# Kernel tuning notes

Hardware: AMD Instinct MI355X
Metric: run time of the kernel (lower is better)

## Reference

```python
import jax, jax.numpy as jnp
import numpy as np
import math

N_EMBD = 384
N_HEAD = 6
HEAD_DIM = N_EMBD // N_HEAD  # 64
EPS = 1e-5


def apply_rotary_emb(x, cos, sin):
    # x: [B, T, H, D]; cos/sin: [1, T, 1, D//2]
    d = x.shape[3] // 2
    x1, x2 = x[..., :d], x[..., d:]
    y1 = x1 * cos + x2 * sin
    y2 = -x1 * sin + x2 * cos
    return jnp.concatenate([y1, y2], axis=3).astype(x.dtype)


def rms_norm(x):
    # no learned gain, eps inside the sqrt's argument as in the torch code
    return x * jax.lax.rsqrt(jnp.mean(x * x, axis=-1, keepdims=True) + EPS)


def setup_inputs() -> dict:
    key = jax.random.key(0)
    ks = jax.random.split(key, 7)
    B, T = 8, 2048
    x = jax.random.normal(ks[0], (B, T, N_EMBD), dtype=jnp.float32)
    scale = 1.0 / math.sqrt(N_EMBD)
    Wq = jax.random.normal(ks[1], (N_EMBD, N_EMBD), dtype=jnp.float32) * scale
    Wk = jax.random.normal(ks[2], (N_EMBD, N_EMBD), dtype=jnp.float32) * scale
    Wv = jax.random.normal(ks[3], (N_EMBD, N_EMBD), dtype=jnp.float32) * scale
    Wo = jax.random.normal(ks[4], (N_EMBD, N_EMBD), dtype=jnp.float32) * scale
    # RoPE tables: true cos/sin of position*inv_freq
    half = HEAD_DIM // 2
    inv_freq = 1.0 / (10000.0 ** (jnp.arange(half, dtype=jnp.float32) / half))
    t = jnp.arange(T, dtype=jnp.float32)
    freqs = t[:, None] * inv_freq[None, :]  # [T, half]
    cos = jnp.cos(freqs)[None, :, None, :]  # [1, T, 1, half]
    sin = jnp.sin(freqs)[None, :, None, :]
    return {"x": x, "Wq": Wq, "Wk": Wk, "Wv": Wv, "Wo": Wo, "cos": cos, "sin": sin}


def reference(x, Wq, Wk, Wv, Wo, cos, sin):
    B, T, C = x.shape
    H, D = N_HEAD, HEAD_DIM
    # torch Linear: y = x @ W.T (weights stored [out, in])
    q = (x @ Wq.T).reshape(B, T, H, D)
    k = (x @ Wk.T).reshape(B, T, H, D)
    v = (x @ Wv.T).reshape(B, T, H, D)
    q = apply_rotary_emb(q, cos, sin)
    k = apply_rotary_emb(k, cos, sin)
    q = rms_norm(q)
    k = rms_norm(k)
    # attention: [B, H, T, T] scores, full softmax (no causal mask in source)
    att = jnp.einsum("bthd,bshd->bhts", q, k) * (1.0 / math.sqrt(D))
    att = jax.nn.softmax(att, axis=-1)
    y = jnp.einsum("bhts,bshd->bthd", att, v).reshape(B, T, C)
    return y @ Wo.T
```

## Files before the change

### kernel.cpp

```cpp
#include <hip/hip_runtime.h>
#include <hip/hip_bf16.h>
#include <stdint.h>

#define B_ 8
#define T_ 2048
#define C_ 384
#define H_ 6
#define D_ 64
#define M_ (B_*T_)

typedef unsigned short u16;
typedef unsigned int u32;
typedef __attribute__((ext_vector_type(8))) short short8;
typedef __attribute__((ext_vector_type(4))) float floatx4;
typedef __attribute__((ext_vector_type(16))) float floatx16;

#define QSCALE 0.18033688011112042f

__device__ __forceinline__ u16 f2b(float f) {
  union { float f; unsigned u; } x; x.f = f;
  unsigned r = x.u + 0x7fffu + ((x.u >> 16) & 1u);
  return (u16)(r >> 16);
}
__device__ __forceinline__ u32 pack_bf16(float a, float b) {
  union { __hip_bfloat162 h; u32 u; } x;
  x.h = __float22bfloat162_rn(float2{a, b});
  return x.u;
}
__device__ __forceinline__ uint4 pack8(const float4& lo, const float4& hi) {
  uint4 r;
  r.x = pack_bf16(lo.x, lo.y); r.y = pack_bf16(lo.z, lo.w);
  r.z = pack_bf16(hi.x, hi.y); r.w = pack_bf16(hi.z, hi.w);
  return r;
}

__device__ __forceinline__ void plswap(u32& a, u32& b) {
  asm("v_permlane32_swap_b32 %0, %1" : "+v"(a), "+v"(b));
}

__device__ __forceinline__ float fexp2(float x) {
#if __has_builtin(__builtin_amdgcn_exp2f)
  return __builtin_amdgcn_exp2f(x);
#else
  float r; asm("v_exp_f32 %0, %1" : "=v"(r) : "v"(x)); return r;
#endif
}

__device__ __forceinline__ u32 cvtpk(float a, float b) {
  u32 r; asm("v_cvt_pk_bf16_f32 %0, %1, %2" : "=v"(r) : "v"(a), "v"(b)); return r;
}

__device__ __forceinline__ void gl_lds16(const u16* g, u16* l) {
#if __has_builtin(__builtin_amdgcn_global_load_lds)
  __builtin_amdgcn_global_load_lds(
      (const __attribute__((address_space(1))) unsigned int*)g,
      (__attribute__((address_space(3))) unsigned int*)l,
      16, 0, 0);
#else
  *reinterpret_cast<uint4*>(l + (threadIdx.x & 63) * 8) =
      *reinterpret_cast<const uint4*>(g);
#endif
}

__global__ __launch_bounds__(256) void prep_bf16(
    const float* __restrict__ x,
    const float* __restrict__ wq, const float* __restrict__ wk,
    const float* __restrict__ wv, const float* __restrict__ wo,
    u16* __restrict__ xb,
    u16* __restrict__ wqb, u16* __restrict__ wkb,
    u16* __restrict__ wvb, u16* __restrict__ wob)
{
  const int c = blockIdx.x * 256 + threadIdx.x;
  const float* src;
  u16* dst;
  int off;
  if (c < 786432) {
    src = x; dst = xb; off = c;
  } else {
    int t = c - 786432;
    int wsel = t / 18432;
    off = t - wsel * 18432;
    src = (wsel == 0) ? wq : (wsel == 1) ? wk : (wsel == 2) ? wv : wo;
    dst = (wsel == 0) ? wqb : (wsel == 1) ? wkb : (wsel == 2) ? wvb : wob;
  }
  const float4* p = reinterpret_cast<const float4*>(src + (size_t)off * 8);
  float4 lo = p[0], hi = p[1];
  *reinterpret_cast<uint4*>(dst + (size_t)off * 8) = pack8(lo, hi);
}

#define QKV_SBUF 10240

__global__ __launch_bounds__(256, 3) void qkv_fused(
    const u16* __restrict__ Xb,
    const u16* __restrict__ Wqb, const u16* __restrict__ Wkb, const u16* __restrict__ Wvb,
    const float* __restrict__ cosb, const float* __restrict__ sinb,
    u16* __restrict__ Qo, u16* __restrict__ Ko, u16* __restrict__ Vto)
{
  __shared__ __align__(16) u16 smem[2 * QKV_SBUF];

  const int id = blockIdx.x;
  const int xcd = id & 7;
  const int s = id >> 3;
  const int mb = xcd * 16 + s / 6;
  const int hh = s % 6;
  const int m0 = mb * 128;
  const int n0 = hh * 64;

  const int tid = threadIdx.x;
  const int w = tid >> 6;
  const int lane = tid & 63;
  const int quad = lane >> 4;
  const int c = lane & 15;

  const u16* Wz[3] = {Wqb, Wkb, Wvb};

  floatx4 acc[3][2][4];
#pragma unroll
  for (int z = 0; z < 3; z++)
#pragma unroll
    for (int i = 0; i < 2; i++)
#pragma unroll
      for (int j = 0; j < 4; j++) acc[z][i][j] = (floatx4){0.f, 0.f, 0.f, 0.f};

  const int lrow = lane >> 2;
  const int lcol = (lane & 3) * 8;

  auto STAGE = [&](int bb, int k0) {
    u16* base = smem + bb * QKV_SBUF;
#pragma unroll
    for (int n = 0; n < 2; n++) {
      const int ch = w * 2 + n;
      gl_lds16(Xb + (size_t)(m0 + ch * 16 + lrow) * C_ + k0 + lcol, base + ch * 512);
    }
#pragma unroll
    for (int n = 0; n < 3; n++) {
      const int idx = w * 3 + n;
      const int z = idx >> 2;
      const int chz = idx & 3;
      gl_lds16(Wz[z] + (size_t)(n0 + chz * 16 + lrow) * C_ + k0 + lcol,
               base + 4096 + z * 2048 + chz * 512);
    }
  };

  STAGE(0, 0);
  __syncthreads();

  for (int i = 0; i < 12; i++) {
    const int bb = i & 1;
    if (i < 11) STAGE(bb ^ 1, (i + 1) * 32);

    const u16* As = smem + bb * QKV_SBUF;
    const u16* Bs0 = As + 4096;
    __builtin_amdgcn_s_setprio(1);
    short8 af2[2];
#pragma unroll
    for (int mi = 0; mi < 2; mi++)
      af2[mi] = *reinterpret_cast<const short8*>(
          As + (w * 32 + mi * 16 + c) * 32 + quad * 8);
#pragma unroll
    for (int z = 0; z < 3; z++) {
#pragma unroll
      for (int ni = 0; ni < 4; ni++) {
        short8 bf = *reinterpret_cast<const short8*>(
            Bs0 + z * 2048 + (ni * 16 + c) * 32 + quad * 8);
#pragma unroll
        for (int mi = 0; mi < 2; mi++)
          acc[z][mi][ni] = __builtin_amdgcn_mfma_f32_16x16x32_bf16(af2[mi], bf, acc[z][mi][ni], 0, 0, 0);
      }
    }
    __builtin_amdgcn_s_setprio(0);
    if (i < 11) __syncthreads();
  }

  const int bb2 = m0 >> 11;
  const int tbase = m0 & (T_ - 1);

  {
    const size_t vbase = ((size_t)(bb2 * H_ + hh)) * D_ * T_;
#pragma unroll
    for (int mi = 0; mi < 2; mi++) {
      int t = tbase + w * 32 + mi * 16 + quad * 4;
#pragma unroll
      for (int ni = 0; ni < 4; ni++) {
        int d = ni * 16 + c;
        ushort4 pk;
        pk.x = f2b(acc[2][mi][ni][0]); pk.y = f2b(acc[2][mi][ni][1]);
        pk.z = f2b(acc[2][mi][ni][2]); pk.w = f2b(acc[2][mi][ni][3]);
        *reinterpret_cast<ushort4*>(Vto + vbase + (size_t)d * T_ + t) = pk;
      }
    }
  }

  u16* Ep = smem;
#pragma unroll
  for (int zz = 0; zz < 2; zz++) {
    __syncthreads();
#pragma unroll
    for (int mi = 0; mi < 2; mi++) {
      float ssr[4];
#pragma unroll
      for (int r = 0; r < 4; r++) {
        float s0 = acc[zz][mi][0][r], s1 = acc[zz][mi][1][r];
        float s2 = acc[zz][mi][2][r], s3 = acc[zz][mi][3][r];
        ssr[r] = s0 * s0 + s1 * s1 + s2 * s2 + s3 * s3;
      }
#pragma unroll
      for (int off = 1; off < 16; off <<= 1)
#pragma unroll
        for (int r = 0; r < 4; r++) ssr[r] += __shfl_xor(ssr[r], off, 64);
      int rowb = w * 32 + mi * 16 + quad * 4;
#pragma unroll
      for (int r = 0; r < 4; r++) {
        float scl = rsqrtf(ssr[r] * (1.0f / 64.0f) + 1e-5f);
        if (zz == 0) scl *= QSCALE;
        int t = tbase + rowb + r;
#pragma unroll
        for (int h2 = 0; h2 < 2; h2++) {
          float cs = cosb[t * 32 + h2 * 16 + c];
          float sn = sinb[t * 32 + h2 * 16 + c];
          float x1 = acc[zz][mi][h2][r];
          float x2 = acc[zz][mi][h2 + 2][r];
          Ep[(rowb + r) * 72 + h2 * 16 + c]       = f2b((x1 * cs + x2 * sn) * scl);
          Ep[(rowb + r) * 72 + (h2 + 2) * 16 + c] = f2b((x2 * cs - x1 * sn) * scl);
        }
      }
    }
    __syncthreads();
    {
      int row = tid >> 1, half = tid & 1;
      int t = tbase + row;
      u16* Og = (zz == 0) ? Qo : Ko;
      u16* dst = Og + (((size_t)(bb2 * H_ + hh)) * T_ + t) * D_ + half * 32;
#pragma unroll
      for (int i = 0; i < 4; i++)
        *reinterpret_cast<uint4*>(dst + i * 8) =
            *reinterpret_cast<const uint4*>(Ep + row * 72 + half * 32 + i * 8);
    }
  }
}

#define ATT_LDA 72
#define ATT_VOFF 4608
#define ATT_BUF 9216

__global__ __launch_bounds__(256, 3) void attn_mfma(
    const u16* __restrict__ Qg, const u16* __restrict__ Kg,
    const u16* __restrict__ Vtg, u16* __restrict__ Yg)
{
  __shared__ __align__(16) u16 smem[2 * ATT_BUF];

  const int tid = threadIdx.x;
  const int w = tid >> 6;
  const int lane = tid & 63;
  const int hi = lane >> 5;
  const int lq = lane & 31;

  const int id = blockIdx.x;
  const int xcd = id & 7;
  const int slot = id >> 3;
  const int bh = xcd * 6 + (slot >> 4);
  const int q0 = (slot & 15) * 128;

  const size_t baseQK = (size_t)bh * T_ * D_;
  const size_t baseV  = (size_t)bh * D_ * T_;

  short8 qf[4];
  {
    const u16* qp = Qg + baseQK + (size_t)(q0 + w * 32 + lq) * D_ + hi * 8;
#pragma unroll
    for (int d = 0; d < 4; d++)
      qf[d] = *reinterpret_cast<const short8*>(qp + d * 16);
  }

  floatx16 z16;
#pragma unroll
  for (int i = 0; i < 16; i++) z16[i] = 0.f;
  short8 vones;
#pragma unroll
  for (int i = 0; i < 8; i++) vones[i] = (short)0x3F80;

  const int sr = tid >> 2;
  const int sch = tid & 3;
  const int ko0 = sr * ATT_LDA + sch * 8;
  const int ko1 = sr * ATT_LDA + (sch + 4) * 8;
  const int vo0 = ATT_VOFF + ko0;
  const int vo1 = ATT_VOFF + ko1;
  const u16* kga = Kg + baseQK + (size_t)sr * D_ + sch * 8;
  const u16* vga = Vtg + baseV + (size_t)sr * T_ + sch * 8;

  uint4 ka = *reinterpret_cast<const uint4*>(kga);
  uint4 kb = *reinterpret_cast<const uint4*>(kga + 32);
  uint4 va = *reinterpret_cast<const uint4*>(vga);
  uint4 vb = *reinterpret_cast<const uint4*>(vga + 32);
  *reinterpret_cast<uint4*>(smem + ko0) = ka;
  *reinterpret_cast<uint4*>(smem + ko1) = kb;
  *reinterpret_cast<uint4*>(smem + vo0) = va;
  *reinterpret_cast<uint4*>(smem + vo1) = vb;
  const u16* kload = kga + (size_t)64 * D_;
  const u16* vload = vga + 64;
  ka = *reinterpret_cast<const uint4*>(kload);
  kb = *reinterpret_cast<const uint4*>(kload + 32);
  va = *reinterpret_cast<const uint4*>(vload);
  vb = *reinterpret_cast<const uint4*>(vload + 32);
  kload += (size_t)64 * D_;
  vload += 64;

  floatx16 o0 = z16, o1 = z16;
  floatx16 l_acc = z16;

  int koff[2][4], voff[2][4];
#pragma unroll
  for (int ds = 0; ds < 4; ds++) {
    const int xr = ds * 2 + hi;
    koff[0][ds] = lq * ATT_LDA + xr * 8;
    koff[1][ds] = (32 + lq) * ATT_LDA + xr * 8;
    voff[0][ds] = ATT_VOFF + lq * ATT_LDA + xr * 8;
    voff[1][ds] = ATT_VOFF + (32 + lq) * ATT_LDA + xr * 8;
  }

  for (int kt = 0; kt < 32; kt++) {
    __syncthreads();

    if (kt < 31) {
      u16* wb = smem + ((kt + 1) & 1) * ATT_BUF;
      *reinterpret_cast<uint4*>(wb + ko0) = ka;
      *reinterpret_cast<uint4*>(wb + ko1) = kb;
      *reinterpret_cast<uint4*>(wb + vo0) = va;
      *reinterpret_cast<uint4*>(wb + vo1) = vb;
      if (kt < 30) {
        ka = *reinterpret_cast<const uint4*>(kload);
        kb = *reinterpret_cast<const uint4*>(kload + 32);
        va = *reinterpret_cast<const uint4*>(vload);
        vb = *reinterpret_cast<const uint4*>(vload + 32);
        kload += (size_t)64 * D_;
        vload += 64;
      }
    }

    const u16* Ksb = smem + (kt & 1) * ATT_BUF;

    floatx16 st0, st1;
    __builtin_amdgcn_s_setprio(1);
    {
      short8 kf0 = *reinterpret_cast<const short8*>(Ksb + koff[0][0]);
      short8 kf1 = *reinterpret_cast<const short8*>(Ksb + koff[1][0]);
      st0 = __builtin_amdgcn_mfma_f32_32x32x16_bf16(kf0, qf[0], z16, 0, 0, 0);
      st1 = __builtin_amdgcn_mfma_f32_32x32x16_bf16(kf1, qf[0], z16, 0, 0, 0);
    }
#pragma unroll
    for (int ds = 1; ds < 4; ds++) {
      short8 kf0 = *reinterpret_cast<const short8*>(Ksb + koff[0][ds]);
      short8 kf1 = *reinterpret_cast<const short8*>(Ksb + koff[1][ds]);
      st0 = __builtin_amdgcn_mfma_f32_32x32x16_bf16(kf0, qf[ds], st0, 0, 0, 0);
      st1 = __builtin_amdgcn_mfma_f32_32x32x16_bf16(kf1, qf[ds], st1, 0, 0, 0);
    }
    __builtin_amdgcn_s_setprio(0);

#pragma unroll
    for (int r = 0; r < 16; r++) {
      st0[r] = fexp2(st0[r]);
      st1[r] = fexp2(st1[r]);
    }

    short8 pa[4];
#pragma unroll
    for (int ks = 0; ks < 4; ks++) {
      const floatx16& s = (ks < 2) ? st0 : st1;
      const int rb = (ks & 1) * 8;
      u32 ca = cvtpk(s[rb + 0], s[rb + 1]);
      u32 cb = cvtpk(s[rb + 2], s[rb + 3]);
      u32 cc = cvtpk(s[rb + 4], s[rb + 5]);
      u32 cd = cvtpk(s[rb + 6], s[rb + 7]);
      plswap(ca, cc);
      plswap(cb, cd);
      short8 pf;
      u32* pfu = reinterpret_cast<u32*>(&pf);
      pfu[0] = ca; pfu[1] = cb; pfu[2] = cc; pfu[3] = cd;
      pa[ks] = pf;
    }

    __builtin_amdgcn_s_setprio(1);
#pragma unroll
    for (int ks = 0; ks < 4; ks++) {
      short8 vf0 = *reinterpret_cast<const short8*>(Ksb + voff[0][ks]);
      short8 vf1 = *reinterpret_cast<const short8*>(Ksb + voff[1][ks]);
      o0 = __builtin_amdgcn_mfma_f32_32x32x16_bf16(pa[ks], vf0, o0, 0, 0, 0);
      o1 = __builtin_amdgcn_mfma_f32_32x32x16_bf16(pa[ks], vf1, o1, 0, 0, 0);
      l_acc = __builtin_amdgcn_mfma_f32_32x32x16_bf16(pa[ks], vones, l_acc, 0, 0, 0);
    }
    __builtin_amdgcn_s_setprio(0);
  }

  float invr[16];
#pragma unroll
  for (int r = 0; r < 16; r++) invr[r] = __builtin_amdgcn_rcpf(l_acc[r]);

  __syncthreads();
  u16* Ep = smem + w * (32 * 72);
#pragma unroll
  for (int nt = 0; nt < 2; nt++) {
    const floatx16& o = nt ? o1 : o0;
#pragma unroll
    for (int r = 0; r < 16; r++) {
      const int rl = (r & 3) + 8 * (r >> 2) + 4 * hi;
      Ep[rl * 72 + nt * 32 + lq] = f2b(o[r] * invr[r]);
    }
  }
  __syncthreads();
  {
    const int row = tid >> 1, half = tid & 1;
    const u16* src = smem + (row >> 5) * (32 * 72) + (row & 31) * 72 + half * 32;
    const int t = q0 + row;
    const int b = bh / H_, h = bh % H_;
    const size_t yi = ((size_t)b * T_ + t) * C_ + (size_t)h * 64 + half * 32;
#pragma unroll
    for (int i = 0; i < 4; i++)
      *reinterpret_cast<uint4*>(Yg + yi + i * 8) =
          *reinterpret_cast<const uint4*>(src + i * 8);
  }
}

#define OUT_SBUF 6144

__global__ __launch_bounds__(256, 4) void out_mfma(
    const u16* __restrict__ Xb, const u16* __restrict__ Wfb, float* __restrict__ Og)
{
  __shared__ __align__(16) u16 smem[17408];

  const int id = blockIdx.x;
  const int xcd = id & 7;
  const int s = id >> 3;
  const int m0 = (xcd * 16 + s / 6) * 128;
  const int n0 = (s % 6) * 64;

  const int tid = threadIdx.x;
  const int w = tid >> 6;
  const int lane = tid & 63;
  const int quad = lane >> 4;
  const int c = lane & 15;

  floatx4 acc[2][4];
#pragma unroll
  for (int i = 0; i < 2; i++)
#pragma unroll
    for (int j = 0; j < 4; j++) acc[i][j] = (floatx4){0.f, 0.f, 0.f, 0.f};

  const int lrow = lane >> 2;
  const int lcol = (lane & 3) * 8;

  auto STAGE = [&](int bb, int k0) {
    u16* base = smem + bb * OUT_SBUF;
#pragma unroll
    for (int n = 0; n < 2; n++) {
      const int ch = w * 2 + n;
      gl_lds16(Xb + (size_t)(m0 + ch * 16 + lrow) * C_ + k0 + lcol, base + ch * 512);
    }
    gl_lds16(Wfb + (size_t)(n0 + w * 16 + lrow) * C_ + k0 + lcol,
             base + 4096 + w * 512);
  };

  STAGE(0, 0);
  __syncthreads();

  for (int i = 0; i < 12; i++) {
    const int bb = i & 1;
    if (i < 11) STAGE(bb ^ 1, (i + 1) * 32);

    const u16* As = smem + bb * OUT_SBUF;
    const u16* Bs = As + 4096;
    __builtin_amdgcn_s_setprio(1);
    short8 af[2], bf[4];
#pragma unroll
    for (int mi = 0; mi < 2; mi++)
      af[mi] = *reinterpret_cast<const short8*>(
          As + (w * 32 + mi * 16 + c) * 32 + quad * 8);
#pragma unroll
    for (int ni = 0; ni < 4; ni++)
      bf[ni] = *reinterpret_cast<const short8*>(
          Bs + (ni * 16 + c) * 32 + quad * 8);
#pragma unroll
    for (int mi = 0; mi < 2; mi++)
#pragma unroll
      for (int ni = 0; ni < 4; ni++)
        acc[mi][ni] = __builtin_amdgcn_mfma_f32_16x16x32_bf16(af[mi], bf[ni], acc[mi][ni], 0, 0, 0);
    __builtin_amdgcn_s_setprio(0);
    if (i < 11) __syncthreads();
  }

  __syncthreads();
  float* Ep = reinterpret_cast<float*>(smem) + w * (32 * 68);
#pragma unroll
  for (int mi = 0; mi < 2; mi++)
#pragma unroll
    for (int ni = 0; ni < 4; ni++) {
      int rw = mi * 16 + quad * 4;
      int col = ni * 16 + c;
#pragma unroll
      for (int r = 0; r < 4; r++)
        Ep[(rw + r) * 68 + col] = acc[mi][ni][r];
    }
  __syncthreads();
  {
    int rw2 = lane >> 1, half = lane & 1;
    const float* src = Ep + rw2 * 68 + half * 32;
    float* dst = Og + (size_t)(m0 + w * 32 + rw2) * C_ + n0 + half * 32;
#pragma unroll
    for (int i = 0; i < 8; i++)
      *reinterpret_cast<float4*>(dst + i * 4) =
          *reinterpret_cast<const float4*>(src + i * 4);
  }
}

extern "C" void kernel_launch(void* const* d_in, const int* in_sizes, int n_in,
                              void* d_out, int out_size, void* d_ws, size_t ws_size,
                              hipStream_t stream) {
  (void)in_sizes; (void)n_in; (void)out_size; (void)ws_size;
  const float* x    = (const float*)d_in[0];
  const float* Wq   = (const float*)d_in[1];
  const float* Wk   = (const float*)d_in[2];
  const float* Wv   = (const float*)d_in[3];
  const float* Wo   = (const float*)d_in[4];
  const float* cosb = (const float*)d_in[5];
  const float* sinb = (const float*)d_in[6];

  const size_t MC = (size_t)M_ * C_;
  u16* ws = (u16*)d_ws;
  u16* Q   = ws;
  u16* K   = Q + MC;
  u16* Vt  = K + MC;
  u16* Y   = Vt + MC;
  u16* Xb  = Y;
  u16* Wb  = Y + MC;
  u16* Wqb = Wb;
  u16* Wkb = Wb + 147456;
  u16* Wvb = Wb + 2 * 147456;
  u16* Wob = Wb + 3 * 147456;
  float* out = (float*)d_out;

  prep_bf16<<<3360, 256, 0, stream>>>(x, Wq, Wk, Wv, Wo, Xb, Wqb, Wkb, Wvb, Wob);

  qkv_fused<<<768, 256, 0, stream>>>(Xb, Wqb, Wkb, Wvb, cosb, sinb, Q, K, Vt);

  attn_mfma<<<768, 256, 0, stream>>>(Q, K, Vt, Y);

  out_mfma<<<768, 256, 0, stream>>>(Y, Wob, out);
}
```

Before: 196.2 us.

## Keep two stages in flight in QKV and output GEMM loops with partial vmcnt waits

The QKV and output projection GEMMs now issue loads for two k-steps up front. Each iteration waits with a partial s_waitcnt vmcnt instead of a full __syncthreads drain, so the next stage's global-to-LDS loads stay outstanding while the current stage computes. After compute, a raw barrier guards buffer reuse before the next stage is refilled. This is meant to hide global load latency better, but correctness now depends on hand-counted vmcnt values matching the number of loads each STAGE issues.

```diff
diff --git a/kernel.cpp b/kernel.cpp
--- a/kernel.cpp
+++ b/kernel.cpp
@@ -60,6 +60,14 @@
   *reinterpret_cast<uint4*>(l + (threadIdx.x & 63) * 8) =
       *reinterpret_cast<const uint4*>(g);
 #endif
+}
+
+__device__ __forceinline__ void rawbar() {
+  __builtin_amdgcn_sched_barrier(0);
+  asm volatile("" ::: "memory");
+  __builtin_amdgcn_s_barrier();
+  asm volatile("" ::: "memory");
+  __builtin_amdgcn_sched_barrier(0);
 }
 
 __global__ __launch_bounds__(256) void prep_bf16(
@@ -143,13 +151,14 @@
   };
 
   STAGE(0, 0);
-  __syncthreads();
+  STAGE(1, 32);
 
   for (int i = 0; i < 12; i++) {
-    const int bb = i & 1;
-    if (i < 11) STAGE(bb ^ 1, (i + 1) * 32);
-
-    const u16* As = smem + bb * QKV_SBUF;
+    if (i < 11) asm volatile("s_waitcnt vmcnt(5)" ::: "memory");
+    else        asm volatile("s_waitcnt vmcnt(0)" ::: "memory");
+    rawbar();
+
+    const u16* As = smem + (i & 1) * QKV_SBUF;
     const u16* Bs0 = As + 4096;
     __builtin_amdgcn_s_setprio(1);
     short8 af2[2];
@@ -169,7 +178,9 @@
       }
     }
     __builtin_amdgcn_s_setprio(0);
-    if (i < 11) __syncthreads();
+
+    rawbar();
+    if (i + 2 < 12) STAGE(i & 1, (i + 2) * 32);
   }
 
   const int bb2 = m0 >> 11;
@@ -460,13 +471,14 @@
   };
 
   STAGE(0, 0);
-  __syncthreads();
+  STAGE(1, 32);
 
   for (int i = 0; i < 12; i++) {
-    const int bb = i & 1;
-    if (i < 11) STAGE(bb ^ 1, (i + 1) * 32);
-
-    const u16* As = smem + bb * OUT_SBUF;
+    if (i < 11) asm volatile("s_waitcnt vmcnt(3)" ::: "memory");
+    else        asm volatile("s_waitcnt vmcnt(0)" ::: "memory");
+    rawbar();
+
+    const u16* As = smem + (i & 1) * OUT_SBUF;
     const u16* Bs = As + 4096;
     __builtin_amdgcn_s_setprio(1);
     short8 af[2], bf[4];
@@ -484,7 +496,9 @@
       for (int ni = 0; ni < 4; ni++)
         acc[mi][ni] = __builtin_amdgcn_mfma_f32_16x16x32_bf16(af[mi], bf[ni], acc[mi][ni], 0, 0, 0);
     __builtin_amdgcn_s_setprio(0);
-    if (i < 11) __syncthreads();
+
+    rawbar();
+    if (i + 2 < 12) STAGE(i & 1, (i + 2) * 32);
   }
 
   __syncthreads();
```

After: 192.2 us. 2.1% less time.
